# Optimization experiments

Measured on AMD Instinct MI355X. Metric: run time of the kernel, lower is better.

## Reference

```python
import jax, jax.numpy as jnp
import numpy as np
from jax import lax

B, S, DIM, H, D = 8, 256, 64, 2, 100
TEMP = 10.0
EPS = 1e-5

def _conv(x, W, b):
    # Conv2d with kernel (H,1), VALID padding, NCHW layout
    y = lax.conv_general_dilated(x, W, (1, 1), 'VALID',
                                 dimension_numbers=('NCHW', 'OIHW', 'NCHW'))
    return y + b[None, :, None, None]

def _bn(x, g, b, m, v):
    # BatchNorm2d in inference mode (running stats)
    scale = (g / jnp.sqrt(v + EPS))[None, :, None, None]
    return (x - m[None, :, None, None]) * scale + b[None, :, None, None]

def setup_inputs() -> dict:
    key = jax.random.key(0)
    ks = jax.random.split(key, 12)
    p = lambda k, sh, s=0.05: jax.random.normal(k, sh, jnp.float32) * s
    return {
        'q': jax.random.normal(ks[0], (B, S, DIM), jnp.float32),
        'k': jax.random.normal(ks[1], (B, S, DIM), jnp.float32),
        'v': jax.random.normal(ks[2], (B, S, DIM), jnp.float32),
        'W1': p(ks[3], (D, 2 * DIM, H, 1)), 'b1': p(ks[4], (D,)),
        'g1': jnp.ones((D,), jnp.float32), 'be1': jnp.zeros((D,), jnp.float32),
        'm1': p(ks[5], (D,)), 'var1': jnp.ones((D,), jnp.float32),
        'W2': p(ks[6], (D, D, H, 1)), 'b2': p(ks[7], (D,)),
        'g2': jnp.ones((D,), jnp.float32), 'be2': jnp.zeros((D,), jnp.float32),
        'm2': p(ks[8], (D,)), 'var2': jnp.ones((D,), jnp.float32),
        'W3': p(ks[9], (1, D, H, 1)), 'b3': p(ks[10], (1,)),
    }

def reference(q, k, v, W1, b1, g1, be1, m1, var1, W2, b2, g2, be2, m2, var2, W3, b3):
    Bq, Sq, T = q.shape
    # q -> (B,T,S,1) broadcast over keys; k -> (B,T,1,S) broadcast over queries
    qe = jnp.broadcast_to(q.transpose(0, 2, 1)[:, :, :, None], (Bq, T, Sq, Sq))
    ke = jnp.broadcast_to(k.transpose(0, 2, 1)[:, :, None, :], (Bq, T, Sq, Sq))
    a = jnp.concatenate([qe, ke], axis=1)            # (B, 2T, S, S)
    a = _conv(a, W1, b1)                             # (B, D, S-H+1, S)
    res = a
    a = jnp.pad(a, ((0, 0), (0, 0), (H - 1, 0), (0, 0)))  # pad height back to S
    a = _bn(a, g1, be1, m1, var1)
    a = _conv(jax.nn.relu(a), W2, b2)                # (B, D, S-H+1, S)
    a = _bn(a + res, g2, be2, m2, var2)
    a = _conv(jax.nn.relu(a), W3, b3)                # (B, 1, S-2H+2, S)
    a = a[:, 0] / TEMP                               # (B, S-2H+2, S)
    attn = jax.nn.softmax(a, axis=2)
    out = jnp.matmul(attn, v)                        # (B, S-2H+2, T)
    return out, attn
```

## Files before the change

kernel.cpp:

```cpp
#include <hip/hip_runtime.h>
#include <hip/hip_bf16.h>

typedef float floatx4 __attribute__((ext_vector_type(4)));
typedef short bhalf8  __attribute__((ext_vector_type(8)));
typedef unsigned short ush;
typedef unsigned int uint;

#define EPS 1e-5f

constexpr int Bb = 8, S = 256, T = 64, Dc = 100;
constexpr int SH = 255;
constexpr int SO = 254;
constexpr int CK = 128;
constexpr int CR = 112;
constexpr int LSTR = 136;

constexpr size_t OFF_U1   = 0;
constexpr size_t OFF_S2   = 512;
constexpr size_t OFF_W30  = 1024;
constexpr size_t OFF_W31  = 1536;
constexpr size_t OFF_W2P  = 2048;
constexpr size_t OFF_AQS  = OFF_W2P + 57344;
constexpr size_t OFF_AQE  = OFF_AQS + (size_t)Bb*SH*CK*4;
constexpr size_t OFF_AKF  = OFF_AQE + (size_t)Bb*SH*CK*4;
constexpr size_t OFF_AKEF = OFF_AKF + (size_t)Bb*16*4*64*8*4;
constexpr size_t OFF_Z0   = OFF_AKEF + (size_t)Bb*16*7*64*4*4;
constexpr size_t OFF_Z1   = OFF_Z0 + (size_t)Bb*SH*S*4;

constexpr int NAQT = 256;
constexpr int NAKT = 256;
constexpr int NW2  = 224;

__device__ __forceinline__ uint pkbf(float lo, float hi) {
    uint a = __float_as_uint(lo) + 0x8000u;
    uint b = __float_as_uint(hi) + 0x8000u;
    return __builtin_amdgcn_perm(b, a, 0x07060302u);
}

__global__ __launch_bounds__(128) void k_prep(const float* __restrict__ q, const float* __restrict__ kin,
                                              const float* __restrict__ W1, const float* __restrict__ b1,
                                              const float* __restrict__ g1, const float* __restrict__ be1,
                                              const float* __restrict__ m1, const float* __restrict__ var1,
                                              const float* __restrict__ W2, const float* __restrict__ b2,
                                              const float* __restrict__ g2, const float* __restrict__ be2,
                                              const float* __restrict__ m2, const float* __restrict__ var2,
                                              const float* __restrict__ W3,
                                              ush* __restrict__ W2p,
                                              float* __restrict__ U1, float* __restrict__ S2,
                                              float* __restrict__ W30, float* __restrict__ W31,
                                              float* __restrict__ AqS, float* __restrict__ AqE,
                                              float* __restrict__ AkF, float* __restrict__ AkEF) {
    __shared__ float sh[100 * 129 + 9 * 64];
    float* xs = sh + 100 * 129;
    const int bid = blockIdx.x, c = threadIdx.x;

    if (bid >= NAQT + NAKT) {
        int r = bid - NAQT - NAKT;
        if (r < NW2) {
            int idx = r * 128 + c;
            int h = idx / (CR * CK);
            int rem = idx % (CR * CK);
            int cc = rem / CK, cp = rem % CK;
            float v = (cc < Dc && cp < Dc) ? W2[((size_t)cc * Dc + cp) * 2 + h] : 0.f;
            __hip_bfloat16 bv = __float2bfloat16(v);
            W2p[idx] = *reinterpret_cast<ush*>(&bv);
        } else {
            float u1 = 0.f, s2 = 0.f, w0 = 0.f, w1 = 0.f;
            if (c < Dc) {
                float sg1 = g1[c] / sqrtf(var1[c] + EPS);
                u1 = be1[c] - m1[c] * sg1;
                s2 = g2[c] / sqrtf(var2[c] + EPS);
                w0 = W3[c * 2 + 0];
                w1 = W3[c * 2 + 1];
            }
            U1[c] = u1; S2[c] = s2; W30[c] = w0; W31[c] = w1;
        }
        return;
    }

    float s1 = 0.f, u1 = 0.f, s2 = 0.f, u2 = 0.f;
    if (c < Dc) {
        s1 = g1[c] / sqrtf(var1[c] + EPS);
        u1 = be1[c] - m1[c] * s1;
        s2 = g2[c] / sqrtf(var2[c] + EPS);
        u2 = (b2[c] - m2[c]) * s2 + be2[c];
    }

    if (bid < NAQT) {
        const int tile = bid & 31, b = bid >> 5;
        const int i0 = tile * 8;
        const int nr = (i0 + 8 <= SH) ? 8 : (SH - i0);
        for (int idx = c; idx < 100 * 128; idx += 128) {
            int cc = idx >> 7, k = idx & 127;
            sh[cc * 129 + k] = W1[(size_t)cc * 256 + k];
        }
        for (int idx = c; idx < (nr + 1) * 64; idx += 128)
            xs[idx] = q[((size_t)b * S + i0 + (idx >> 6)) * T + (idx & 63)];
        __syncthreads();
        float acc[8] = {0.f, 0.f, 0.f, 0.f, 0.f, 0.f, 0.f, 0.f};
        if (c < Dc) {
            const float* wr = sh + c * 129;
            #pragma unroll 2
            for (int t = 0; t < 64; ++t) {
                const float w0 = wr[2 * t], w1 = wr[2 * t + 1];
                #pragma unroll
                for (int r = 0; r < 8; ++r)
                    acc[r] = fmaf(xs[r * 64 + t], w0, fmaf(xs[(r + 1) * 64 + t], w1, acc[r]));
            }
        }
        const float b1v = (c < Dc) ? b1[c] : 0.f;
        for (int r = 0; r < nr; ++r) {
            float s = (c < Dc) ? (acc[r] + b1v) : 0.f;
            size_t row = ((size_t)b * SH + i0 + r) * CK + c;
            AqS[row] = s * s1 + u1;
            AqE[row] = s * s2 + u2;
        }
    } else {
        const int r0 = bid - NAQT;
        const int tile = r0 & 31, b = r0 >> 5;
        const int j0 = tile * 8;
        for (int idx = c; idx < 100 * 64; idx += 128) {
            int cc = idx >> 6, t = idx & 63;
            const float2 p = reinterpret_cast<const float2*>(W1 + (size_t)cc * 256 + 128)[t];
            sh[cc * 129 + t] = p.x + p.y;
        }
        for (int idx = c; idx < 8 * 64; idx += 128)
            xs[idx] = kin[((size_t)b * S + j0 + (idx >> 6)) * T + (idx & 63)];
        __syncthreads();
        float acc[8] = {0.f, 0.f, 0.f, 0.f, 0.f, 0.f, 0.f, 0.f};
        if (c < Dc) {
            const float* wr = sh + c * 129;
            #pragma unroll 2
            for (int t = 0; t < 64; ++t) {
                const float w = wr[t];
                #pragma unroll
                for (int r = 0; r < 8; ++r)
                    acc[r] = fmaf(xs[r * 64 + t], w, acc[r]);
            }
        }
        const int ks = c >> 5, qq = (c >> 3) & 3, e = c & 7;
        const int ct = c >> 4, q2 = (c >> 2) & 3, rr2 = c & 3;
        #pragma unroll
        for (int r = 0; r < 8; ++r) {
            const int j = j0 + r;
            const int j16 = j >> 4, ln = j & 15;
            const float s = (c < Dc) ? acc[r] : 0.f;
            AkF[((((size_t)b * 16 + j16) * 4 + ks) * 64 + qq * 16 + ln) * 8 + e] = s * s1;
            if (c < 112)
                AkEF[((((size_t)b * 16 + j16) * 7 + ct) * 64 + q2 * 16 + ln) * 4 + rr2] = s * s2;
        }
    }
}

__global__ __launch_bounds__(512, 4) void k_main(const float* __restrict__ AqS, const float* __restrict__ AqE,
                                                 const float* __restrict__ AkF, const float* __restrict__ AkEF,
                                                 const ush* __restrict__ W2p,
                                                 const float* __restrict__ U1, const float* __restrict__ S2,
                                                 const float* __restrict__ W30f, const float* __restrict__ W31f,
                                                 float* __restrict__ Z0, float* __restrict__ Z1) {
    __shared__ __align__(16) ush W2s[2 * CR * LSTR];
    __shared__ __align__(16) float aqsh[2][128];
    const int tid = threadIdx.x;
    const int wv = tid >> 6, lane = tid & 63, ln = lane & 15, quad = lane >> 4;
    const int ip = blockIdx.x, b = blockIdx.y;
    const int j16A = wv << 1;

    floatx4 acc0[7], acc1[7];
    #pragma unroll
    for (int ct = 0; ct < 7; ++ct) {
        acc0[ct] = (floatx4){0.f, 0.f, 0.f, 0.f};
        acc1[ct] = (floatx4){0.f, 0.f, 0.f, 0.f};
    }

    for (int idx = tid; idx < 2 * CR * 16; idx += 512) {
        int row = idx >> 4, ch = idx & 15;
        *reinterpret_cast<uint4*>(&W2s[row * LSTR + ch * 8]) =
            *reinterpret_cast<const uint4*>(&W2p[row * CK + ch * 8]);
    }
    {
        const bool pad0 = (ip == 0);
        const float* aq0 = pad0 ? U1 : (AqS + (size_t)(b * SH + ip - 1) * CK);
        const float* aq1 = AqS + (size_t)(b * SH + ip) * CK;
        if (tid < 256) {
            const float* src = (tid < 128) ? aq0 : aq1;
            aqsh[tid >> 7][tid & 127] = src[tid & 127];
        }
    }
    __syncthreads();

    const float m0 = (ip == 0) ? 0.f : 1.f;
    const float* fA = AkF + ((size_t)(b * 16 + j16A) * 4 * 64 + lane) * 8;
    const float* fB = fA + 4 * 64 * 8;

    float4 ka = *reinterpret_cast<const float4*>(fA);
    float4 kb = *reinterpret_cast<const float4*>(fA + 4);
    float4 kc = *reinterpret_cast<const float4*>(fB);
    float4 kd = *reinterpret_cast<const float4*>(fB + 4);

    #pragma unroll 1
    for (int ks = 0; ks < 4; ++ks) {
        const int k0 = ks * 32 + quad * 8;
        const int kn = ((ks + 1) & 3) * 512;
        const float4 ka2 = *reinterpret_cast<const float4*>(fA + kn);
        const float4 kb2 = *reinterpret_cast<const float4*>(fA + kn + 4);
        const float4 kc2 = *reinterpret_cast<const float4*>(fB + kn);
        const float4 kd2 = *reinterpret_cast<const float4*>(fB + kn + 4);
        {
            const float4 qa = *reinterpret_cast<const float4*>(&aqsh[0][k0]);
            const float4 qb = *reinterpret_cast<const float4*>(&aqsh[0][k0 + 4]);
            uint4 p, rr;
            p.x  = pkbf(fmaxf(fmaf(ka.x, m0, qa.x), 0.f), fmaxf(fmaf(ka.y, m0, qa.y), 0.f));
            p.y  = pkbf(fmaxf(fmaf(ka.z, m0, qa.z), 0.f), fmaxf(fmaf(ka.w, m0, qa.w), 0.f));
            p.z  = pkbf(fmaxf(fmaf(kb.x, m0, qb.x), 0.f), fmaxf(fmaf(kb.y, m0, qb.y), 0.f));
            p.w  = pkbf(fmaxf(fmaf(kb.z, m0, qb.z), 0.f), fmaxf(fmaf(kb.w, m0, qb.w), 0.f));
            rr.x = pkbf(fmaxf(fmaf(kc.x, m0, qa.x), 0.f), fmaxf(fmaf(kc.y, m0, qa.y), 0.f));
            rr.y = pkbf(fmaxf(fmaf(kc.z, m0, qa.z), 0.f), fmaxf(fmaf(kc.w, m0, qa.w), 0.f));
            rr.z = pkbf(fmaxf(fmaf(kd.x, m0, qb.x), 0.f), fmaxf(fmaf(kd.y, m0, qb.y), 0.f));
            rr.w = pkbf(fmaxf(fmaf(kd.z, m0, qb.z), 0.f), fmaxf(fmaf(kd.w, m0, qb.w), 0.f));
            const bhalf8 bf0 = *reinterpret_cast<bhalf8*>(&p);
            const bhalf8 bf1 = *reinterpret_cast<bhalf8*>(&rr);
            #pragma unroll
            for (int ct = 0; ct < 7; ++ct) {
                const bhalf8 af = *reinterpret_cast<const bhalf8*>(&W2s[(ct * 16 + ln) * LSTR + k0]);
                acc0[ct] = __builtin_amdgcn_mfma_f32_16x16x32_bf16(af, bf0, acc0[ct], 0, 0, 0);
                acc1[ct] = __builtin_amdgcn_mfma_f32_16x16x32_bf16(af, bf1, acc1[ct], 0, 0, 0);
            }
        }
        {
            const float4 qa = *reinterpret_cast<const float4*>(&aqsh[1][k0]);
            const float4 qb = *reinterpret_cast<const float4*>(&aqsh[1][k0 + 4]);
            uint4 p, rr;
            p.x  = pkbf(fmaxf(qa.x + ka.x, 0.f), fmaxf(qa.y + ka.y, 0.f));
            p.y  = pkbf(fmaxf(qa.z + ka.z, 0.f), fmaxf(qa.w + ka.w, 0.f));
            p.z  = pkbf(fmaxf(qb.x + kb.x, 0.f), fmaxf(qb.y + kb.y, 0.f));
            p.w  = pkbf(fmaxf(qb.z + kb.z, 0.f), fmaxf(qb.w + kb.w, 0.f));
            rr.x = pkbf(fmaxf(qa.x + kc.x, 0.f), fmaxf(qa.y + kc.y, 0.f));
            rr.y = pkbf(fmaxf(qa.z + kc.z, 0.f), fmaxf(qa.w + kc.w, 0.f));
            rr.z = pkbf(fmaxf(qb.x + kd.x, 0.f), fmaxf(qb.y + kd.y, 0.f));
            rr.w = pkbf(fmaxf(qb.z + kd.z, 0.f), fmaxf(qb.w + kd.w, 0.f));
            const bhalf8 bf0 = *reinterpret_cast<bhalf8*>(&p);
            const bhalf8 bf1 = *reinterpret_cast<bhalf8*>(&rr);
            #pragma unroll
            for (int ct = 0; ct < 7; ++ct) {
                const bhalf8 af = *reinterpret_cast<const bhalf8*>(&W2s[(CR + ct * 16 + ln) * LSTR + k0]);
                acc0[ct] = __builtin_amdgcn_mfma_f32_16x16x32_bf16(af, bf0, acc0[ct], 0, 0, 0);
                acc1[ct] = __builtin_amdgcn_mfma_f32_16x16x32_bf16(af, bf1, acc1[ct], 0, 0, 0);
            }
        }
        ka = ka2; kb = kb2; kc = kc2; kd = kd2;
    }

    float z0a = 0.f, z1a = 0.f, z0b = 0.f, z1b = 0.f;
    const float* aqer = AqE + (size_t)(b * SH + ip) * CK;
    const float* eA = AkEF + ((size_t)(b * 16 + j16A) * 7 * 64 + lane) * 4;
    const float* eB = eA + 7 * 64 * 4;
    #pragma unroll
    for (int ct = 0; ct < 7; ++ct) {
        const int c = ct * 16 + (quad << 2);
        const float4 aq  = *reinterpret_cast<const float4*>(aqer + c);
        const float4 aka = *reinterpret_cast<const float4*>(eA + ct * 256);
        const float4 akb = *reinterpret_cast<const float4*>(eB + ct * 256);
        const float4 s2  = *reinterpret_cast<const float4*>(S2 + c);
        const float4 w0  = *reinterpret_cast<const float4*>(W30f + c);
        const float4 w1  = *reinterpret_cast<const float4*>(W31f + c);
        const float aqv[4] = {aq.x, aq.y, aq.z, aq.w};
        const float kav[4] = {aka.x, aka.y, aka.z, aka.w};
        const float kbv[4] = {akb.x, akb.y, akb.z, akb.w};
        const float s2v[4] = {s2.x, s2.y, s2.z, s2.w};
        const float w0v[4] = {w0.x, w0.y, w0.z, w0.w};
        const float w1v[4] = {w1.x, w1.y, w1.z, w1.w};
        #pragma unroll
        for (int r = 0; r < 4; ++r) {
            float ta = fmaxf(fmaf(acc0[ct][r], s2v[r], aqv[r] + kav[r]), 0.f);
            z0a = fmaf(ta, w0v[r], z0a);
            z1a = fmaf(ta, w1v[r], z1a);
            float tb = fmaxf(fmaf(acc1[ct][r], s2v[r], aqv[r] + kbv[r]), 0.f);
            z0b = fmaf(tb, w0v[r], z0b);
            z1b = fmaf(tb, w1v[r], z1b);
        }
    }
    z0a += __shfl_xor(z0a, 16, 64); z0a += __shfl_xor(z0a, 32, 64);
    z1a += __shfl_xor(z1a, 16, 64); z1a += __shfl_xor(z1a, 32, 64);
    z0b += __shfl_xor(z0b, 16, 64); z0b += __shfl_xor(z0b, 32, 64);
    z1b += __shfl_xor(z1b, 16, 64); z1b += __shfl_xor(z1b, 32, 64);
    if (lane < 16) {
        size_t zi = (size_t)(b * SH + ip) * S + wv * 32 + lane;
        Z0[zi] = z0a; Z1[zi] = z1a;
        Z0[zi + 16] = z0b; Z1[zi + 16] = z1b;
    }
}

__global__ __launch_bounds__(256) void k_soft(const float* __restrict__ Z0, const float* __restrict__ Z1,
                                              const float* __restrict__ v,
                                              const float* __restrict__ b3,
                                              float* __restrict__ outp,
                                              float* __restrict__ attnp) {
    __shared__ float attn_s[4][256];
    const int wv = threadIdx.x >> 6, lane = threadIdx.x & 63;
    const int i = blockIdx.x * 4 + wv;
    const int b = blockIdx.y;
    if (i >= SO) return;
    const float b3f = b3[0];
    const size_t zr = (size_t)(b * SH + i) * S;
    const float4 z0 = *reinterpret_cast<const float4*>(Z0 + zr + lane * 4);
    const float4 z1 = *reinterpret_cast<const float4*>(Z1 + zr + S + lane * 4);
    float l0 = (z0.x + z1.x + b3f) * 0.1f;
    float l1 = (z0.y + z1.y + b3f) * 0.1f;
    float l2 = (z0.z + z1.z + b3f) * 0.1f;
    float l3 = (z0.w + z1.w + b3f) * 0.1f;

    float mx = fmaxf(fmaxf(l0, l1), fmaxf(l2, l3));
    #pragma unroll
    for (int o = 1; o < 64; o <<= 1) mx = fmaxf(mx, __shfl_xor(mx, o, 64));
    float e0 = __expf(l0 - mx), e1 = __expf(l1 - mx), e2 = __expf(l2 - mx), e3 = __expf(l3 - mx);
    float sm = e0 + e1 + e2 + e3;
    #pragma unroll
    for (int o = 1; o < 64; o <<= 1) sm += __shfl_xor(sm, o, 64);
    const float inv = 1.f / sm;
    const float a0 = e0 * inv, a1 = e1 * inv, a2 = e2 * inv, a3 = e3 * inv;
    *reinterpret_cast<float4*>(attnp + (size_t)(b * SO + i) * S + lane * 4) = make_float4(a0, a1, a2, a3);
    *reinterpret_cast<float4*>(&attn_s[wv][lane * 4]) = make_float4(a0, a1, a2, a3);

    const float* vb = v + (size_t)b * S * T + lane;
    float p0 = 0.f, p1 = 0.f, p2 = 0.f, p3 = 0.f;
    #pragma unroll 4
    for (int j = 0; j < 256; j += 4) {
        p0 = fmaf(attn_s[wv][j],     vb[(size_t)j * T],       p0);
        p1 = fmaf(attn_s[wv][j + 1], vb[(size_t)(j + 1) * T], p1);
        p2 = fmaf(attn_s[wv][j + 2], vb[(size_t)(j + 2) * T], p2);
        p3 = fmaf(attn_s[wv][j + 3], vb[(size_t)(j + 3) * T], p3);
    }
    outp[(size_t)(b * SO + i) * T + lane] = (p0 + p1) + (p2 + p3);
}

extern "C" void kernel_launch(void* const* d_in, const int* in_sizes, int n_in,
                              void* d_out, int out_size, void* d_ws, size_t ws_size,
                              hipStream_t stream) {
    const float* q    = (const float*)d_in[0];
    const float* kin  = (const float*)d_in[1];
    const float* vin  = (const float*)d_in[2];
    const float* W1   = (const float*)d_in[3];
    const float* b1   = (const float*)d_in[4];
    const float* g1   = (const float*)d_in[5];
    const float* be1  = (const float*)d_in[6];
    const float* m1   = (const float*)d_in[7];
    const float* var1 = (const float*)d_in[8];
    const float* W2   = (const float*)d_in[9];
    const float* b2   = (const float*)d_in[10];
    const float* g2   = (const float*)d_in[11];
    const float* be2  = (const float*)d_in[12];
    const float* m2   = (const float*)d_in[13];
    const float* var2 = (const float*)d_in[14];
    const float* W3   = (const float*)d_in[15];
    const float* b3   = (const float*)d_in[16];

    char* ws = (char*)d_ws;
    float* U1   = (float*)(ws + OFF_U1);
    float* S2p  = (float*)(ws + OFF_S2);
    float* W30  = (float*)(ws + OFF_W30);
    float* W31  = (float*)(ws + OFF_W31);
    ush*   W2p  = (ush*)(ws + OFF_W2P);
    float* AqS  = (float*)(ws + OFF_AQS);
    float* AqE  = (float*)(ws + OFF_AQE);
    float* AkF  = (float*)(ws + OFF_AKF);
    float* AkEF = (float*)(ws + OFF_AKEF);
    float* Z0   = (float*)(ws + OFF_Z0);
    float* Z1   = (float*)(ws + OFF_Z1);

    float* outp  = (float*)d_out;
    float* attnp = outp + (size_t)Bb * SO * T;

    k_prep<<<NAQT + NAKT + NW2 + 1, 128, 0, stream>>>(q, kin, W1, b1, g1, be1, m1, var1,
                                                      W2, b2, g2, be2, m2, var2, W3,
                                                      W2p, U1, S2p, W30, W31,
                                                      AqS, AqE, AkF, AkEF);
    k_main<<<dim3(SH, Bb), 512, 0, stream>>>(AqS, AqE, AkF, AkEF, W2p, U1, S2p, W30, W31, Z0, Z1);
    k_soft<<<dim3((SO + 3) / 4, Bb), 256, 0, stream>>>(Z0, Z1, vin, b3, outp, attnp);
}
```

Before: 159.5 us.

## Tile main kernel over two query rows sharing the middle conv row

Each block of the main kernel now computes two adjacent output rows for half of the key columns, instead of one row for all columns. The middle relu'd layer-1 row feeds both the second tap of the first row and the first tap of the second row, so three B fragments are built per k-step instead of four per pair. This cuts elementwise packing work and per-row loads of the key features. The grid roughly halves in blocks along rows and doubles along columns, so the W2 shared-memory fill per block is amortized over different work; row 255 is clamped and masked.

Result: slower. 166.3 us (+4.3%).

```diff
diff --git a/kernel.cpp b/kernel.cpp
--- a/kernel.cpp
+++ b/kernel.cpp
@@ -159,11 +159,12 @@
                                                  const float* __restrict__ W30f, const float* __restrict__ W31f,
                                                  float* __restrict__ Z0, float* __restrict__ Z1) {
     __shared__ __align__(16) ush W2s[2 * CR * LSTR];
-    __shared__ __align__(16) float aqsh[2][128];
+    __shared__ __align__(16) float aqsh[3][128];
     const int tid = threadIdx.x;
     const int wv = tid >> 6, lane = tid & 63, ln = lane & 15, quad = lane >> 4;
-    const int ip = blockIdx.x, b = blockIdx.y;
-    const int j16A = wv << 1;
+    const int rp = blockIdx.x, jt = blockIdx.y, b = blockIdx.z;
+    const int i0 = rp * 2;
+    const int j16 = jt * 8 + wv;
 
     floatx4 acc0[7], acc1[7];
     #pragma unroll
@@ -177,25 +178,24 @@
         *reinterpret_cast<uint4*>(&W2s[row * LSTR + ch * 8]) =
             *reinterpret_cast<const uint4*>(&W2p[row * CK + ch * 8]);
     }
-    {
-        const bool pad0 = (ip == 0);
-        const float* aq0 = pad0 ? U1 : (AqS + (size_t)(b * SH + ip - 1) * CK);
-        const float* aq1 = AqS + (size_t)(b * SH + ip) * CK;
-        if (tid < 256) {
-            const float* src = (tid < 128) ? aq0 : aq1;
-            aqsh[tid >> 7][tid & 127] = src[tid & 127];
-        }
+    if (tid < 384) {
+        int r = tid >> 7, cc = tid & 127;
+        int gi = i0 - 1 + r;
+        const float* src;
+        if (gi < 0) src = U1;
+        else {
+            if (gi > SH - 1) gi = SH - 1;
+            src = AqS + (size_t)(b * SH + gi) * CK;
+        }
+        aqsh[r][cc] = src[cc];
     }
     __syncthreads();
 
-    const float m0 = (ip == 0) ? 0.f : 1.f;
-    const float* fA = AkF + ((size_t)(b * 16 + j16A) * 4 * 64 + lane) * 8;
-    const float* fB = fA + 4 * 64 * 8;
+    const float m0 = (i0 == 0) ? 0.f : 1.f;
+    const float* fA = AkF + ((size_t)(b * 16 + j16) * 4 * 64 + lane) * 8;
 
     float4 ka = *reinterpret_cast<const float4*>(fA);
     float4 kb = *reinterpret_cast<const float4*>(fA + 4);
-    float4 kc = *reinterpret_cast<const float4*>(fB);
-    float4 kd = *reinterpret_cast<const float4*>(fB + 4);
 
     #pragma unroll 1
     for (int ks = 0; ks < 4; ++ks) {
@@ -203,90 +203,82 @@
         const int kn = ((ks + 1) & 3) * 512;
         const float4 ka2 = *reinterpret_cast<const float4*>(fA + kn);
         const float4 kb2 = *reinterpret_cast<const float4*>(fA + kn + 4);
-        const float4 kc2 = *reinterpret_cast<const float4*>(fB + kn);
-        const float4 kd2 = *reinterpret_cast<const float4*>(fB + kn + 4);
+
+        uint4 pm, p0, pp;
         {
             const float4 qa = *reinterpret_cast<const float4*>(&aqsh[0][k0]);
             const float4 qb = *reinterpret_cast<const float4*>(&aqsh[0][k0 + 4]);
-            uint4 p, rr;
-            p.x  = pkbf(fmaxf(fmaf(ka.x, m0, qa.x), 0.f), fmaxf(fmaf(ka.y, m0, qa.y), 0.f));
-            p.y  = pkbf(fmaxf(fmaf(ka.z, m0, qa.z), 0.f), fmaxf(fmaf(ka.w, m0, qa.w), 0.f));
-            p.z  = pkbf(fmaxf(fmaf(kb.x, m0, qb.x), 0.f), fmaxf(fmaf(kb.y, m0, qb.y), 0.f));
-            p.w  = pkbf(fmaxf(fmaf(kb.z, m0, qb.z), 0.f), fmaxf(fmaf(kb.w, m0, qb.w), 0.f));
-            rr.x = pkbf(fmaxf(fmaf(kc.x, m0, qa.x), 0.f), fmaxf(fmaf(kc.y, m0, qa.y), 0.f));
-            rr.y = pkbf(fmaxf(fmaf(kc.z, m0, qa.z), 0.f), fmaxf(fmaf(kc.w, m0, qa.w), 0.f));
-            rr.z = pkbf(fmaxf(fmaf(kd.x, m0, qb.x), 0.f), fmaxf(fmaf(kd.y, m0, qb.y), 0.f));
-            rr.w = pkbf(fmaxf(fmaf(kd.z, m0, qb.z), 0.f), fmaxf(fmaf(kd.w, m0, qb.w), 0.f));
-            const bhalf8 bf0 = *reinterpret_cast<bhalf8*>(&p);
-            const bhalf8 bf1 = *reinterpret_cast<bhalf8*>(&rr);
-            #pragma unroll
-            for (int ct = 0; ct < 7; ++ct) {
-                const bhalf8 af = *reinterpret_cast<const bhalf8*>(&W2s[(ct * 16 + ln) * LSTR + k0]);
-                acc0[ct] = __builtin_amdgcn_mfma_f32_16x16x32_bf16(af, bf0, acc0[ct], 0, 0, 0);
-                acc1[ct] = __builtin_amdgcn_mfma_f32_16x16x32_bf16(af, bf1, acc1[ct], 0, 0, 0);
-            }
+            pm.x = pkbf(fmaxf(fmaf(ka.x, m0, qa.x), 0.f), fmaxf(fmaf(ka.y, m0, qa.y), 0.f));
+            pm.y = pkbf(fmaxf(fmaf(ka.z, m0, qa.z), 0.f), fmaxf(fmaf(ka.w, m0, qa.w), 0.f));
+            pm.z = pkbf(fmaxf(fmaf(kb.x, m0, qb.x), 0.f), fmaxf(fmaf(kb.y, m0, qb.y), 0.f));
+            pm.w = pkbf(fmaxf(fmaf(kb.z, m0, qb.z), 0.f), fmaxf(fmaf(kb.w, m0, qb.w), 0.f));
         }
         {
             const float4 qa = *reinterpret_cast<const float4*>(&aqsh[1][k0]);
             const float4 qb = *reinterpret_cast<const float4*>(&aqsh[1][k0 + 4]);
-            uint4 p, rr;
-            p.x  = pkbf(fmaxf(qa.x + ka.x, 0.f), fmaxf(qa.y + ka.y, 0.f));
-            p.y  = pkbf(fmaxf(qa.z + ka.z, 0.f), fmaxf(qa.w + ka.w, 0.f));
-            p.z  = pkbf(fmaxf(qb.x + kb.x, 0.f), fmaxf(qb.y + kb.y, 0.f));
-            p.w  = pkbf(fmaxf(qb.z + kb.z, 0.f), fmaxf(qb.w + kb.w, 0.f));
-            rr.x = pkbf(fmaxf(qa.x + kc.x, 0.f), fmaxf(qa.y + kc.y, 0.f));
-            rr.y = pkbf(fmaxf(qa.z + kc.z, 0.f), fmaxf(qa.w + kc.w, 0.f));
-            rr.z = pkbf(fmaxf(qb.x + kd.x, 0.f), fmaxf(qb.y + kd.y, 0.f));
-            rr.w = pkbf(fmaxf(qb.z + kd.z, 0.f), fmaxf(qb.w + kd.w, 0.f));
-            const bhalf8 bf0 = *reinterpret_cast<bhalf8*>(&p);
-            const bhalf8 bf1 = *reinterpret_cast<bhalf8*>(&rr);
+            p0.x = pkbf(fmaxf(qa.x + ka.x, 0.f), fmaxf(qa.y + ka.y, 0.f));
+            p0.y = pkbf(fmaxf(qa.z + ka.z, 0.f), fmaxf(qa.w + ka.w, 0.f));
+            p0.z = pkbf(fmaxf(qb.x + kb.x, 0.f), fmaxf(qb.y + kb.y, 0.f));
+            p0.w = pkbf(fmaxf(qb.z + kb.z, 0.f), fmaxf(qb.w + kb.w, 0.f));
+        }
+        {
+            const float4 qa = *reinterpret_cast<const float4*>(&aqsh[2][k0]);
+            const float4 qb = *reinterpret_cast<const float4*>(&aqsh[2][k0 + 4]);
+            pp.x = pkbf(fmaxf(qa.x + ka.x, 0.f), fmaxf(qa.y + ka.y, 0.f));
+            pp.y = pkbf(fmaxf(qa.z + ka.z, 0.f), fmaxf(qa.w + ka.w, 0.f));
+            pp.z = pkbf(fmaxf(qb.x + kb.x, 0.f), fmaxf(qb.y + kb.y, 0.f));
+            pp.w = pkbf(fmaxf(qb.z + kb.z, 0.f), fmaxf(qb.w + kb.w, 0.f));
+        }
+        const bhalf8 fm1 = *reinterpret_cast<bhalf8*>(&pm);
+        const bhalf8 f0  = *reinterpret_cast<bhalf8*>(&p0);
+        const bhalf8 fp1 = *reinterpret_cast<bhalf8*>(&pp);
+
+        #pragma unroll
+        for (int ct = 0; ct < 7; ++ct) {
+            const bhalf8 af0 = *reinterpret_cast<const bhalf8*>(&W2s[(ct * 16 + ln) * LSTR + k0]);
+            const bhalf8 af1 = *reinterpret_cast<const bhalf8*>(&W2s[(CR + ct * 16 + ln) * LSTR + k0]);
+            acc0[ct] = __builtin_amdgcn_mfma_f32_16x16x32_bf16(af0, fm1, acc0[ct], 0, 0, 0);
+            acc0[ct] = __builtin_amdgcn_mfma_f32_16x16x32_bf16(af1, f0,  acc0[ct], 0, 0, 0);
+            acc1[ct] = __builtin_amdgcn_mfma_f32_16x16x32_bf16(af0, f0,  acc1[ct], 0, 0, 0);
+            acc1[ct] = __builtin_amdgcn_mfma_f32_16x16x32_bf16(af1, fp1, acc1[ct], 0, 0, 0);
+        }
+        ka = ka2; kb = kb2;
+    }
+
+    const float* eA = AkEF + ((size_t)(b * 16 + j16) * 7 * 64 + lane) * 4;
+    #pragma unroll
+    for (int row = 0; row < 2; ++row) {
+        const int gi = i0 + row;
+        const int gic = (gi < SH) ? gi : (SH - 1);
+        const float* aqer = AqE + (size_t)(b * SH + gic) * CK;
+        const floatx4* acc = row ? acc1 : acc0;
+        float z0 = 0.f, z1 = 0.f;
+        #pragma unroll
+        for (int ct = 0; ct < 7; ++ct) {
+            const int c = ct * 16 + (quad << 2);
+            const float4 aq  = *reinterpret_cast<const float4*>(aqer + c);
+            const float4 ake = *reinterpret_cast<const float4*>(eA + ct * 256);
+            const float4 s2  = *reinterpret_cast<const float4*>(S2 + c);
+            const float4 w0  = *reinterpret_cast<const float4*>(W30f + c);
+            const float4 w1  = *reinterpret_cast<const float4*>(W31f + c);
+            const float aqv[4] = {aq.x, aq.y, aq.z, aq.w};
+            const float kev[4] = {ake.x, ake.y, ake.z, ake.w};
+            const float s2v[4] = {s2.x, s2.y, s2.z, s2.w};
+            const float w0v[4] = {w0.x, w0.y, w0.z, w0.w};
+            const float w1v[4] = {w1.x, w1.y, w1.z, w1.w};
             #pragma unroll
-            for (int ct = 0; ct < 7; ++ct) {
-                const bhalf8 af = *reinterpret_cast<const bhalf8*>(&W2s[(CR + ct * 16 + ln) * LSTR + k0]);
-                acc0[ct] = __builtin_amdgcn_mfma_f32_16x16x32_bf16(af, bf0, acc0[ct], 0, 0, 0);
-                acc1[ct] = __builtin_amdgcn_mfma_f32_16x16x32_bf16(af, bf1, acc1[ct], 0, 0, 0);
+            for (int r = 0; r < 4; ++r) {
+                float ta = fmaxf(fmaf(acc[ct][r], s2v[r], aqv[r] + kev[r]), 0.f);
+                z0 = fmaf(ta, w0v[r], z0);
+                z1 = fmaf(ta, w1v[r], z1);
             }
         }
-        ka = ka2; kb = kb2; kc = kc2; kd = kd2;
-    }
-
-    float z0a = 0.f, z1a = 0.f, z0b = 0.f, z1b = 0.f;
-    const float* aqer = AqE + (size_t)(b * SH + ip) * CK;
-    const float* eA = AkEF + ((size_t)(b * 16 + j16A) * 7 * 64 + lane) * 4;
-    const float* eB = eA + 7 * 64 * 4;
-    #pragma unroll
-    for (int ct = 0; ct < 7; ++ct) {
-        const int c = ct * 16 + (quad << 2);
-        const float4 aq  = *reinterpret_cast<const float4*>(aqer + c);
-        const float4 aka = *reinterpret_cast<const float4*>(eA + ct * 256);
-        const float4 akb = *reinterpret_cast<const float4*>(eB + ct * 256);
-        const float4 s2  = *reinterpret_cast<const float4*>(S2 + c);
-        const float4 w0  = *reinterpret_cast<const float4*>(W30f + c);
-        const float4 w1  = *reinterpret_cast<const float4*>(W31f + c);
-        const float aqv[4] = {aq.x, aq.y, aq.z, aq.w};
-        const float kav[4] = {aka.x, aka.y, aka.z, aka.w};
-        const float kbv[4] = {akb.x, akb.y, akb.z, akb.w};
-        const float s2v[4] = {s2.x, s2.y, s2.z, s2.w};
-        const float w0v[4] = {w0.x, w0.y, w0.z, w0.w};
-        const float w1v[4] = {w1.x, w1.y, w1.z, w1.w};
-        #pragma unroll
-        for (int r = 0; r < 4; ++r) {
-            float ta = fmaxf(fmaf(acc0[ct][r], s2v[r], aqv[r] + kav[r]), 0.f);
-            z0a = fmaf(ta, w0v[r], z0a);
-            z1a = fmaf(ta, w1v[r], z1a);
-            float tb = fmaxf(fmaf(acc1[ct][r], s2v[r], aqv[r] + kbv[r]), 0.f);
-            z0b = fmaf(tb, w0v[r], z0b);
-            z1b = fmaf(tb, w1v[r], z1b);
-        }
-    }
-    z0a += __shfl_xor(z0a, 16, 64); z0a += __shfl_xor(z0a, 32, 64);
-    z1a += __shfl_xor(z1a, 16, 64); z1a += __shfl_xor(z1a, 32, 64);
-    z0b += __shfl_xor(z0b, 16, 64); z0b += __shfl_xor(z0b, 32, 64);
-    z1b += __shfl_xor(z1b, 16, 64); z1b += __shfl_xor(z1b, 32, 64);
-    if (lane < 16) {
-        size_t zi = (size_t)(b * SH + ip) * S + wv * 32 + lane;
-        Z0[zi] = z0a; Z1[zi] = z1a;
-        Z0[zi + 16] = z0b; Z1[zi + 16] = z1b;
+        z0 += __shfl_xor(z0, 16, 64); z0 += __shfl_xor(z0, 32, 64);
+        z1 += __shfl_xor(z1, 16, 64); z1 += __shfl_xor(z1, 32, 64);
+        if (lane < 16 && gi < SH) {
+            size_t zi = (size_t)(b * SH + gi) * S + j16 * 16 + lane;
+            Z0[zi] = z0; Z1[zi] = z1;
+        }
     }
 }
 
@@ -374,6 +366,6 @@
                                                       W2, b2, g2, be2, m2, var2, W3,
                                                       W2p, U1, S2p, W30, W31,
                                                       AqS, AqE, AkF, AkEF);
-    k_main<<<dim3(SH, Bb), 512, 0, stream>>>(AqS, AqE, AkF, AkEF, W2p, U1, S2p, W30, W31, Z0, Z1);
+    k_main<<<dim3(128, 2, Bb), 512, 0, stream>>>(AqS, AqE, AkF, AkEF, W2p, U1, S2p, W30, W31, Z0, Z1);
     k_soft<<<dim3((SO + 3) / 4, Bb), 256, 0, stream>>>(Z0, Z1, vin, b3, outp, attnp);
 }
```
